# Performance work log

Measured on AMD Instinct MI355X. Metric: run time of the kernel, lower is better.

The kernel has to match this reference:

```python
import jax, jax.numpy as jnp
import numpy as np

B, T, C = 8, 1024, 768
H = 12
D = C // H  # 64


def rope_tables(seq_len, head_dim, dtype=jnp.float32):
    inv_freq = 1.0 / (10000.0 ** (jnp.arange(0, head_dim, 2, dtype=jnp.float32) / head_dim))
    t = jnp.arange(seq_len, dtype=jnp.float32)
    freqs = jnp.outer(t, inv_freq)            # [T, D/2]
    emb = jnp.concatenate([freqs, freqs], -1)  # [T, D]
    return jnp.cos(emb).astype(dtype), jnp.sin(emb).astype(dtype)


def rotate_half(x):
    x1, x2 = jnp.split(x, 2, axis=-1)
    return jnp.concatenate([-x2, x1], axis=-1)


def setup_inputs() -> dict:
    key = jax.random.key(0)
    k1, k2, k3 = jax.random.split(key, 3)
    x = jax.random.normal(k1, (B, T, C), dtype=jnp.float32)
    w_qkv = jax.random.normal(k2, (3 * C, C), dtype=jnp.float32) * (1.0 / np.sqrt(C))
    w_proj = jax.random.normal(k3, (C, C), dtype=jnp.float32) * (1.0 / np.sqrt(C))
    return {"x": x, "w_qkv": w_qkv, "w_proj": w_proj}


def reference(x, w_qkv, w_proj):
    b, t, c = x.shape
    qkv = jnp.einsum('btc,oc->bto', x, w_qkv)            # [B,T,3C]
    qkv = qkv.reshape(b, t, 3, H, D)
    q = qkv[:, :, 0].transpose(0, 2, 1, 3)               # [B,H,T,D]
    k = qkv[:, :, 1].transpose(0, 2, 1, 3)
    v = qkv[:, :, 2].transpose(0, 2, 1, 3)

    cos, sin = rope_tables(t, D, x.dtype)                # [T,D]
    cos = cos[None, None]                                # [1,1,T,D]
    sin = sin[None, None]
    q = q * cos + rotate_half(q) * sin
    k = k * cos + rotate_half(k) * sin

    scale = 1.0 / np.sqrt(D)
    scores = jnp.einsum('bhqd,bhkd->bhqk', q, k) * scale  # [B,H,T,T]
    causal = jnp.tril(jnp.ones((t, t), dtype=bool))
    scores = jnp.where(causal[None, None], scores, jnp.finfo(scores.dtype).min)
    attn = jax.nn.softmax(scores, axis=-1)
    out = jnp.einsum('bhqk,bhkd->bhqd', attn, v)          # [B,H,T,D]
    out = out.transpose(0, 2, 1, 3).reshape(b, t, c)      # [B,T,C]
    return jnp.einsum('btc,oc->bto', out, w_proj)
```

## Files before the change

kernel.cpp:

```cpp
#include <hip/hip_runtime.h>
#include <hip/hip_bf16.h>
#include <math.h>

#define B_ 8
#define T_ 1024
#define C_ 768
#define H_ 12
#define D_ 64
#define THREEC 2304

typedef short short8 __attribute__((ext_vector_type(8)));
typedef float f32x4 __attribute__((ext_vector_type(4)));

__device__ inline f32x4 mfma16(short8 a, short8 b, f32x4 c) {
    asm("v_mfma_f32_16x16x32_bf16 %0, %1, %2, %0" : "+v"(c) : "v"(a), "v"(b));
    return c;
}

#define GLOAD16(gp, lp)                                                        \
    __builtin_amdgcn_global_load_lds(                                          \
        (const __attribute__((address_space(1))) unsigned int*)(gp),           \
        (__attribute__((address_space(3))) unsigned int*)(lp), 16, 0, 0)

__device__ inline unsigned short f2bf(float f) {
    __hip_bfloat16 h = __float2bfloat16(f);
    return *reinterpret_cast<unsigned short*>(&h);
}
__device__ inline unsigned int pack2bf(float lo, float hi) {
    return (unsigned int)f2bf(lo) | ((unsigned int)f2bf(hi) << 16);
}

__global__ __launch_bounds__(256) void cvt_f32_bf16_kernel(const float* __restrict__ src,
                                                           unsigned short* __restrict__ dst,
                                                           int n4) {
    int i = blockIdx.x * 256 + threadIdx.x;
    if (i >= n4) return;
    float4 v = ((const float4*)src)[i];
    ushort4 o;
    o.x = f2bf(v.x); o.y = f2bf(v.y); o.z = f2bf(v.z); o.w = f2bf(v.w);
    ((ushort4*)dst)[i] = o;
}

__global__ __launch_bounds__(256) void rope_table_kernel(float* __restrict__ cosT,
                                                         float* __restrict__ sinT) {
    int idx = blockIdx.x * 256 + threadIdx.x;
    int t = idx >> 5, i = idx & 31;
    float inv_freq = powf(10000.0f, -(float)i / 32.0f);
    float ang = (float)t * inv_freq;
    cosT[idx] = cosf(ang);
    sinT[idx] = sinf(ang);
}

#define BM 128
#define BN 128
#define BKK 32

__global__ __launch_bounds__(256) void gemm_bt_mfma(const unsigned short* __restrict__ A,
                                                    const unsigned short* __restrict__ Bm,
                                                    float* __restrict__ Cm,
                                                    int M, int N, int K) {
    __shared__ short As[BM * BKK];
    __shared__ short Bs[BN * BKK];

    const int tid = threadIdx.x;
    const int w = tid >> 6, l = tid & 63;
    const int wr = w >> 1, wc = w & 1;
    const int row0 = blockIdx.x * BM, col0 = blockIdx.y * BN;

    const int srow = w * 16 + (l >> 2);
    const int scol = (l & 3) * 8;

    f32x4 acc[4][4];
#pragma unroll
    for (int m = 0; m < 4; ++m)
#pragma unroll
        for (int n = 0; n < 4; ++n) acc[m][n] = (f32x4){0.f, 0.f, 0.f, 0.f};

    const int fr = l & 15;
    const int fk = (l >> 4) * 8;

    for (int k0 = 0; k0 < K; k0 += BKK) {
        __syncthreads();
#pragma unroll
        for (int half = 0; half < 2; ++half) {
            int r = srow + half * 64;
            GLOAD16(&A[(size_t)(row0 + r) * K + k0 + scol], &As[(half * 64 + w * 16) * BKK]);
            GLOAD16(&Bm[(size_t)(col0 + r) * K + k0 + scol], &Bs[(half * 64 + w * 16) * BKK]);
        }
        __syncthreads();

        short8 af[4], bf[4];
#pragma unroll
        for (int m = 0; m < 4; ++m)
            af[m] = *(const short8*)&As[(wr * 64 + m * 16 + fr) * BKK + fk];
#pragma unroll
        for (int n = 0; n < 4; ++n)
            bf[n] = *(const short8*)&Bs[(wc * 64 + n * 16 + fr) * BKK + fk];
#pragma unroll
        for (int m = 0; m < 4; ++m)
#pragma unroll
            for (int n = 0; n < 4; ++n)
                acc[m][n] = mfma16(af[m], bf[n], acc[m][n]);
    }

    const int crow = (l >> 4) * 4;
    const int ccol = l & 15;
#pragma unroll
    for (int m = 0; m < 4; ++m)
#pragma unroll
        for (int n = 0; n < 4; ++n) {
            size_t base = (size_t)(row0 + wr * 64 + m * 16 + crow) * N + col0 + wc * 64 + n * 16 + ccol;
#pragma unroll
            for (int j = 0; j < 4; ++j) Cm[base + (size_t)j * N] = acc[m][n][j];
        }
}

__global__ __launch_bounds__(256) void prep_kernel(const float* __restrict__ qkv,
                                                   const float* __restrict__ cosT,
                                                   const float* __restrict__ sinT,
                                                   unsigned short* __restrict__ Kb,
                                                   unsigned short* __restrict__ VT) {
    const int tt = blockIdx.x, h = blockIdx.y, b = blockIdx.z;
    const int tid = threadIdx.x;
    const int bh = b * H_ + h;
    __shared__ unsigned short Vs[64][68];

#pragma unroll
    for (int p = 0; p < 2; ++p) {
        int tl = p * 32 + (tid >> 3);
        int t = tt * 64 + tl;
        int d0 = (tid & 7) * 4;
        const float* row = qkv + (size_t)(b * T_ + t) * THREEC + C_ + h * D_;
        float4 x0 = *(const float4*)(row + d0);
        float4 x1 = *(const float4*)(row + 32 + d0);
        float4 c = *(const float4*)(cosT + t * 32 + d0);
        float4 s = *(const float4*)(sinT + t * 32 + d0);
        ushort4 o0, o1;
        o0.x = f2bf(x0.x * c.x - x1.x * s.x);  o1.x = f2bf(x1.x * c.x + x0.x * s.x);
        o0.y = f2bf(x0.y * c.y - x1.y * s.y);  o1.y = f2bf(x1.y * c.y + x0.y * s.y);
        o0.z = f2bf(x0.z * c.z - x1.z * s.z);  o1.z = f2bf(x1.z * c.z + x0.z * s.z);
        o0.w = f2bf(x0.w * c.w - x1.w * s.w);  o1.w = f2bf(x1.w * c.w + x0.w * s.w);
        unsigned short* kout = Kb + ((size_t)bh * T_ + t) * D_;
        *(ushort4*)(kout + d0) = o0;
        *(ushort4*)(kout + 32 + d0) = o1;
    }

    {
        int tl = tid >> 2;
        int t = tt * 64 + tl;
        int d0 = (tid & 3) * 16;
        const float* vrow = qkv + (size_t)(b * T_ + t) * THREEC + 2 * C_ + h * D_;
#pragma unroll
        for (int c4 = 0; c4 < 4; ++c4) {
            float4 v = *(const float4*)(vrow + d0 + c4 * 4);
            ushort4 u;
            u.x = f2bf(v.x); u.y = f2bf(v.y); u.z = f2bf(v.z); u.w = f2bf(v.w);
            *(ushort4*)&Vs[tl][d0 + c4 * 4] = u;
        }
    }
    __syncthreads();
    {
        int d = tid >> 2;
        int tc0 = (tid & 3) * 16;
        unsigned short tmp[16];
#pragma unroll
        for (int i = 0; i < 16; ++i) tmp[i] = Vs[tc0 + i][d];
        unsigned short* vout = VT + ((size_t)bh * D_ + d) * T_ + tt * 64 + tc0;
        union { short8 v; unsigned short u[8]; } a0, a1;
#pragma unroll
        for (int i = 0; i < 8; ++i) { a0.u[i] = tmp[i]; a1.u[i] = tmp[8 + i]; }
        *(short8*)vout = a0.v;
        *(short8*)(vout + 8) = a1.v;
    }
}

__global__ __launch_bounds__(256) void attn_mfma_kernel(const float* __restrict__ qkv,
                                                        const unsigned short* __restrict__ Kb,
                                                        const unsigned short* __restrict__ VT,
                                                        const float* __restrict__ cosT,
                                                        const float* __restrict__ sinT,
                                                        unsigned short* __restrict__ ao_bf) {
    const int qblk = blockIdx.x, h = blockIdx.y, b = blockIdx.z;
    const int tid = threadIdx.x;
    const int w = tid >> 6, l = tid & 63;
    const int g = l >> 4, c = l & 15;
    const int bh = b * H_ + h;
    const float scale = 0.125f;

    __shared__ __align__(16) char smem[17408];
    unsigned short* Ks  = (unsigned short*)smem;
    unsigned short* VTs = (unsigned short*)(smem + 8192);
    float* Ot = (float*)smem;

    const int q_g = qblk * 64 + w * 16 + c;

    const float* qrow = qkv + ((size_t)(b * T_) + q_g) * THREEC + h * D_;
    float x0[8], x1[8], cv[8], sv[8];
    *(float4*)&x0[0] = *(const float4*)(qrow + g * 8);
    *(float4*)&x0[4] = *(const float4*)(qrow + g * 8 + 4);
    *(float4*)&x1[0] = *(const float4*)(qrow + 32 + g * 8);
    *(float4*)&x1[4] = *(const float4*)(qrow + 32 + g * 8 + 4);
    *(float4*)&cv[0] = *(const float4*)(cosT + q_g * 32 + g * 8);
    *(float4*)&cv[4] = *(const float4*)(cosT + q_g * 32 + g * 8 + 4);
    *(float4*)&sv[0] = *(const float4*)(sinT + q_g * 32 + g * 8);
    *(float4*)&sv[4] = *(const float4*)(sinT + q_g * 32 + g * 8 + 4);
    union { short8 v; unsigned short u[8]; } qa0, qa1;
#pragma unroll
    for (int j = 0; j < 8; ++j) {
        qa0.u[j] = f2bf(x0[j] * cv[j] - x1[j] * sv[j]);
        qa1.u[j] = f2bf(x1[j] * cv[j] + x0[j] * sv[j]);
    }

    f32x4 o[4];
#pragma unroll
    for (int db = 0; db < 4; ++db) o[db] = (f32x4){0.f, 0.f, 0.f, 0.f};
    float m = -INFINITY, lsum = 0.f;

    const int sswz = ((l & 7) ^ (l >> 3)) * 8;
    const int sw0 = (g ^ (c & 7)) * 8;
    const int sw1 = ((g + 4) ^ (c & 7)) * 8;

    const int ktiles = qblk + 1;
    for (int kt = 0; kt < ktiles; ++kt) {
        __syncthreads();
#pragma unroll
        for (int sub = 0; sub < 2; ++sub) {
            int r = w * 16 + sub * 8 + (l >> 3);
            GLOAD16(Kb + ((size_t)bh * T_ + kt * 64 + r) * D_ + sswz,
                    Ks + (w * 16 + sub * 8) * 64);
            GLOAD16(VT + ((size_t)bh * D_ + r) * T_ + kt * 64 + sswz,
                    VTs + (w * 16 + sub * 8) * 64);
        }
        __syncthreads();

        f32x4 st[4];
#pragma unroll
        for (int t = 0; t < 4; ++t) {
            short8 k0 = *(const short8*)&Ks[(t * 16 + c) * 64 + sw0];
            short8 k1 = *(const short8*)&Ks[(t * 16 + c) * 64 + sw1];
            f32x4 z = (f32x4){0.f, 0.f, 0.f, 0.f};
            z = mfma16(k0, qa0.v, z);
            st[t] = mfma16(k1, qa1.v, z);
        }

        float p[16];
        float tmax = -INFINITY;
#pragma unroll
        for (int t = 0; t < 4; ++t)
#pragma unroll
            for (int j = 0; j < 4; ++j) {
                int kg = kt * 64 + t * 16 + g * 4 + j;
                float v = (kg <= q_g) ? st[t][j] * scale : -INFINITY;
                p[t * 4 + j] = v;
                tmax = fmaxf(tmax, v);
            }
        tmax = fmaxf(tmax, __shfl_xor(tmax, 16));
        tmax = fmaxf(tmax, __shfl_xor(tmax, 32));
        float mnew = fmaxf(m, tmax);
        float corr = __expf(m - mnew);
        m = mnew;
        float psum = 0.f;
#pragma unroll
        for (int i = 0; i < 16; ++i) { p[i] = __expf(p[i] - m); psum += p[i]; }
        psum += __shfl_xor(psum, 16);
        psum += __shfl_xor(psum, 32);
        lsum = lsum * corr + psum;
#pragma unroll
        for (int db = 0; db < 4; ++db)
#pragma unroll
            for (int j = 0; j < 4; ++j) o[db][j] *= corr;

        unsigned int u[4][2];
#pragma unroll
        for (int t = 0; t < 4; ++t) {
            u[t][0] = pack2bf(p[t * 4 + 0], p[t * 4 + 1]);
            u[t][1] = pack2bf(p[t * 4 + 2], p[t * 4 + 3]);
        }

        const int srcA = (((g & 1) << 1) | (g >> 1)) * 16 + c;
        const int srcB = (((g & 1) << 1) | ((g >> 1) ^ 1)) * 16 + c;
        const int hi = g >> 1;
        union { short8 v; unsigned int w[4]; } pb[2];
#pragma unroll
        for (int kb = 0; kb < 2; ++kb)
#pragma unroll
            for (int p2 = 0; p2 < 2; ++p2) {
                unsigned int varA = (g & 1) ? u[kb * 2 + 1][p2] : u[kb * 2][p2];
                unsigned int varB = (g & 1) ? u[kb * 2][p2] : u[kb * 2 + 1][p2];
                unsigned int wA = __shfl(varA, srcA, 64);
                unsigned int wB = __shfl(varB, srcB, 64);
                pb[kb].w[p2]     = hi ? wB : wA;
                pb[kb].w[p2 + 2] = hi ? wA : wB;
            }

#pragma unroll
        for (int db = 0; db < 4; ++db) {
            short8 va0 = *(const short8*)&VTs[(db * 16 + c) * 64 + sw0];
            short8 va1 = *(const short8*)&VTs[(db * 16 + c) * 64 + sw1];
            o[db] = mfma16(va0, pb[0].v, o[db]);
            o[db] = mfma16(va1, pb[1].v, o[db]);
        }
    }

    __syncthreads();
    const float inv = 1.0f / lsum;
    float* ow = Ot + w * 1088;
#pragma unroll
    for (int db = 0; db < 4; ++db)
#pragma unroll
        for (int j = 0; j < 4; ++j)
            ow[c * 68 + db * 16 + g * 4 + j] = o[db][j] * inv;
    __syncthreads();
    {
        const float* orow = ow + c * 68 + g * 16;
        f32x4 v0 = *(const f32x4*)(orow);
        f32x4 v1 = *(const f32x4*)(orow + 4);
        f32x4 v2 = *(const f32x4*)(orow + 8);
        f32x4 v3 = *(const f32x4*)(orow + 12);
        union { short8 v; unsigned int w[4]; } s0, s1;
        s0.w[0] = pack2bf(v0[0], v0[1]); s0.w[1] = pack2bf(v0[2], v0[3]);
        s0.w[2] = pack2bf(v1[0], v1[1]); s0.w[3] = pack2bf(v1[2], v1[3]);
        s1.w[0] = pack2bf(v2[0], v2[1]); s1.w[1] = pack2bf(v2[2], v2[3]);
        s1.w[2] = pack2bf(v3[0], v3[1]); s1.w[3] = pack2bf(v3[2], v3[3]);
        unsigned short* op = ao_bf + ((size_t)(b * T_) + qblk * 64 + w * 16 + c) * C_ + h * D_ + g * 16;
        *(short8*)op = s0.v;
        *(short8*)(op + 8) = s1.v;
    }
}

extern "C" void kernel_launch(void* const* d_in, const int* in_sizes, int n_in,
                              void* d_out, int out_size, void* d_ws, size_t ws_size,
                              hipStream_t stream) {
    const float* x      = (const float*)d_in[0];
    const float* w_qkv  = (const float*)d_in[1];
    const float* w_proj = (const float*)d_in[2];
    float* out = (float*)d_out;

    float* ws   = (float*)d_ws;
    float* qkv  = ws;
    float* cosT = ws + 18874368;
    float* sinT = ws + 18907136;
    unsigned short* x_bf  = (unsigned short*)(ws + 18939904);
    unsigned short* wq_bf = x_bf + 6291456;
    unsigned short* wp_bf = wq_bf + 1769472;
    unsigned short* ao_bf = wp_bf + 589824;
    unsigned short* Kb    = ao_bf + 6291456;
    unsigned short* VT    = Kb + 6291456;

    cvt_f32_bf16_kernel<<<6291456 / 4 / 256, 256, 0, stream>>>(x, x_bf, 6291456 / 4);
    cvt_f32_bf16_kernel<<<1769472 / 4 / 256, 256, 0, stream>>>(w_qkv, wq_bf, 1769472 / 4);
    cvt_f32_bf16_kernel<<<589824 / 4 / 256, 256, 0, stream>>>(w_proj, wp_bf, 589824 / 4);
    rope_table_kernel<<<(T_ * 32) / 256, 256, 0, stream>>>(cosT, sinT);

    gemm_bt_mfma<<<dim3(8192 / BM, 2304 / BN), 256, 0, stream>>>(x_bf, wq_bf, qkv, 8192, 2304, 768);

    prep_kernel<<<dim3(T_ / 64, H_, B_), 256, 0, stream>>>(qkv, cosT, sinT, Kb, VT);

    attn_mfma_kernel<<<dim3(T_ / 64, H_, B_), 256, 0, stream>>>(qkv, Kb, VT, cosT, sinT, ao_bf);

    gemm_bt_mfma<<<dim3(8192 / BM, 768 / BN), 256, 0, stream>>>(ao_bf, wp_bf, out, 8192, 768, 768);
}
```

Baseline: 230.1 us.

## Widen attention blocks to 128 queries with 8 waves and reverse block order

```diff
diff --git a/kernel.cpp b/kernel.cpp
--- a/kernel.cpp
+++ b/kernel.cpp
@@ -174,25 +174,25 @@
     }
 }
 
-__global__ __launch_bounds__(256) void attn_mfma_kernel(const float* __restrict__ qkv,
+#define QBLK 128
+
+__global__ __launch_bounds__(512) void attn_mfma_kernel(const float* __restrict__ qkv,
                                                         const unsigned short* __restrict__ Kb,
                                                         const unsigned short* __restrict__ VT,
                                                         const float* __restrict__ cosT,
                                                         const float* __restrict__ sinT,
                                                         unsigned short* __restrict__ ao_bf) {
-    const int qblk = blockIdx.x, h = blockIdx.y, b = blockIdx.z;
+    const int qblk = (T_ / QBLK - 1) - blockIdx.x;
+    const int h = blockIdx.y, b = blockIdx.z;
     const int tid = threadIdx.x;
     const int w = tid >> 6, l = tid & 63;
     const int g = l >> 4, c = l & 15;
     const int bh = b * H_ + h;
-    const float scale = 0.125f;
-
-    __shared__ __align__(16) char smem[17408];
-    unsigned short* Ks  = (unsigned short*)smem;
-    unsigned short* VTs = (unsigned short*)(smem + 8192);
+
+    __shared__ __align__(16) char smem[34816];
     float* Ot = (float*)smem;
 
-    const int q_g = qblk * 64 + w * 16 + c;
+    const int q_g = qblk * QBLK + w * 16 + c;
 
     const float* qrow = qkv + ((size_t)(b * T_) + q_g) * THREEC + h * D_;
     float x0[8], x1[8], cv[8], sv[8];
@@ -207,8 +207,8 @@
     union { short8 v; unsigned short u[8]; } qa0, qa1;
 #pragma unroll
     for (int j = 0; j < 8; ++j) {
-        qa0.u[j] = f2bf(x0[j] * cv[j] - x1[j] * sv[j]);
-        qa1.u[j] = f2bf(x1[j] * cv[j] + x0[j] * sv[j]);
+        qa0.u[j] = f2bf((x0[j] * cv[j] - x1[j] * sv[j]) * 0.125f);
+        qa1.u[j] = f2bf((x1[j] * cv[j] + x0[j] * sv[j]) * 0.125f);
     }
 
     f32x4 o[4];
@@ -219,19 +219,21 @@
     const int sswz = ((l & 7) ^ (l >> 3)) * 8;
     const int sw0 = (g ^ (c & 7)) * 8;
     const int sw1 = ((g + 4) ^ (c & 7)) * 8;
-
-    const int ktiles = qblk + 1;
+    const int srow = w * 8 + (l >> 3);
+
+    const unsigned short* Ks  = (const unsigned short*)smem;
+    const unsigned short* VTs = (const unsigned short*)(smem + 8192);
+
+    const int ktiles = 2 * qblk + 2;
     for (int kt = 0; kt < ktiles; ++kt) {
         __syncthreads();
-#pragma unroll
-        for (int sub = 0; sub < 2; ++sub) {
-            int r = w * 16 + sub * 8 + (l >> 3);
-            GLOAD16(Kb + ((size_t)bh * T_ + kt * 64 + r) * D_ + sswz,
-                    Ks + (w * 16 + sub * 8) * 64);
-            GLOAD16(VT + ((size_t)bh * D_ + r) * T_ + kt * 64 + sswz,
-                    VTs + (w * 16 + sub * 8) * 64);
-        }
+        GLOAD16(Kb + ((size_t)bh * T_ + kt * 64 + srow) * D_ + sswz,
+                (unsigned short*)smem + (w * 8) * 64);
+        GLOAD16(VT + ((size_t)bh * D_ + srow) * T_ + kt * 64 + sswz,
+                (unsigned short*)(smem + 8192) + (w * 8) * 64);
         __syncthreads();
+
+        if (kt * 64 > qblk * QBLK + w * 16 + 15) continue;
 
         f32x4 st[4];
 #pragma unroll
@@ -245,15 +247,25 @@
 
         float p[16];
         float tmax = -INFINITY;
-#pragma unroll
-        for (int t = 0; t < 4; ++t)
-#pragma unroll
-            for (int j = 0; j < 4; ++j) {
-                int kg = kt * 64 + t * 16 + g * 4 + j;
-                float v = (kg <= q_g) ? st[t][j] * scale : -INFINITY;
-                p[t * 4 + j] = v;
-                tmax = fmaxf(tmax, v);
-            }
+        if (kt * 64 + 63 <= qblk * QBLK + w * 16) {
+#pragma unroll
+            for (int t = 0; t < 4; ++t)
+#pragma unroll
+                for (int j = 0; j < 4; ++j) {
+                    p[t * 4 + j] = st[t][j];
+                    tmax = fmaxf(tmax, st[t][j]);
+                }
+        } else {
+#pragma unroll
+            for (int t = 0; t < 4; ++t)
+#pragma unroll
+                for (int j = 0; j < 4; ++j) {
+                    int kg = kt * 64 + t * 16 + g * 4 + j;
+                    float v = (kg <= q_g) ? st[t][j] : -INFINITY;
+                    p[t * 4 + j] = v;
+                    tmax = fmaxf(tmax, v);
+                }
+        }
         tmax = fmaxf(tmax, __shfl_xor(tmax, 16));
         tmax = fmaxf(tmax, __shfl_xor(tmax, 32));
         float mnew = fmaxf(m, tmax);
@@ -322,7 +334,7 @@
         s0.w[2] = pack2bf(v1[0], v1[1]); s0.w[3] = pack2bf(v1[2], v1[3]);
         s1.w[0] = pack2bf(v2[0], v2[1]); s1.w[1] = pack2bf(v2[2], v2[3]);
         s1.w[2] = pack2bf(v3[0], v3[1]); s1.w[3] = pack2bf(v3[2], v3[3]);
-        unsigned short* op = ao_bf + ((size_t)(b * T_) + qblk * 64 + w * 16 + c) * C_ + h * D_ + g * 16;
+        unsigned short* op = ao_bf + ((size_t)(b * T_) + qblk * QBLK + w * 16 + c) * C_ + h * D_ + g * 16;
         *(short8*)op = s0.v;
         *(short8*)(op + 8) = s1.v;
     }
@@ -356,7 +368,7 @@
 
     prep_kernel<<<dim3(T_ / 64, H_, B_), 256, 0, stream>>>(qkv, cosT, sinT, Kb, VT);
 
-    attn_mfma_kernel<<<dim3(T_ / 64, H_, B_), 256, 0, stream>>>(qkv, Kb, VT, cosT, sinT, ao_bf);
+    attn_mfma_kernel<<<dim3(T_ / QBLK, H_, B_), 512, 0, stream>>>(qkv, Kb, VT, cosT, sinT, ao_bf);
 
     gemm_bt_mfma<<<dim3(8192 / BM, 768 / BN), 256, 0, stream>>>(ao_bf, wp_bf, out, 8192, 768, 768);
 }
```

After: 219.9 us. -4.4%, faster.
